# Performance work log

Measured on AMD Instinct MI355X. Metric: run time of the kernel, lower is better.

Reference implementation:

```python
import jax, jax.numpy as jnp
import numpy as np

VOCAB, D, H, HK, DH, M, DFF, NCLS = 32000, 512, 8, 2, 64, 64, 2048, 2
G = H // HK  # GQA group size = 4
EPS = 1e-6


def rmsnorm(x, g):
    return x * jax.lax.rsqrt(jnp.mean(x * x, axis=-1, keepdims=True) + EPS) * g


def setup_inputs() -> dict:
    key = jax.random.key(0)
    ks = jax.random.split(key, 14)
    s = 0.02
    return {
        "input_ids": jax.random.randint(ks[0], (8, 8192), 0, VOCAB),
        "emb": jax.random.normal(ks[1], (VOCAB, D), jnp.float32) * s,
        "Wq": jax.random.normal(ks[2], (D, H * DH), jnp.float32) * s,
        "Wk": jax.random.normal(ks[3], (D, HK * DH), jnp.float32) * s,
        "Wv": jax.random.normal(ks[4], (D, HK * DH), jnp.float32) * s,
        "Wphi": jax.random.normal(ks[5], (DH, M), jnp.float32),  # Laplacian kernel feature projection
        "Wo": jax.random.normal(ks[6], (H * DH, D), jnp.float32) * s,
        "g1": jnp.ones((D,), jnp.float32),
        "g2": jnp.ones((D,), jnp.float32),
        "Wg": jax.random.normal(ks[7], (D, DFF), jnp.float32) * s,
        "Wu": jax.random.normal(ks[8], (D, DFF), jnp.float32) * s,  # frozen up_proj (freeze only affects training, not math)
        "Wd": jax.random.normal(ks[9], (DFF, D), jnp.float32) * s,
        "Wc": jax.random.normal(ks[10], (D, NCLS), jnp.float32) * s,
        "bc": jnp.zeros((NCLS,), jnp.float32),
    }


def reference(input_ids, emb, Wq, Wk, Wv, Wphi, Wo, g1, g2, Wg, Wu, Wd, Wc, bc):
    B, S = input_ids.shape
    x = emb[input_ids]  # [B,S,D] embedding gather
    # --- kernelized (Laplacian) bidirectional GQA linear attention, pre-norm ---
    h = rmsnorm(x, g1)
    q = (h @ Wq).reshape(B, S, H, DH)
    k = (h @ Wk).reshape(B, S, HK, DH)
    v = (h @ Wv).reshape(B, S, HK, DH)
    # Laplacian positive feature map: phi(u) = exp(-|u @ Wphi|)  -> [.., M]
    pq = jnp.exp(-jnp.abs(jnp.einsum("bshd,dm->bshm", q, Wphi)))
    pk = jnp.exp(-jnp.abs(jnp.einsum("bskd,dm->bskm", k, Wphi)))
    # global (bidirectional) state per kv head: [B,HK,M,DH] and normalizer [B,HK,M]
    kv = jnp.einsum("bskm,bskd->bkmd", pk, v)
    z = pk.sum(axis=1)
    pqg = pq.reshape(B, S, HK, G, M)  # group query heads onto kv heads
    num = jnp.einsum("bskgm,bkmd->bskgd", pqg, kv)
    den = jnp.einsum("bskgm,bkm->bskg", pqg, z)
    attn = (num / (den[..., None] + EPS)).reshape(B, S, H * DH)
    x = x + attn @ Wo
    # --- SwiGLU FFN, pre-norm ---
    h2 = rmsnorm(x, g2)
    x = x + (jax.nn.silu(h2 @ Wg) * (h2 @ Wu)) @ Wd
    # --- mean pool + linear head ---
    logits = x.mean(axis=1) @ Wc + bc  # [B, NCLS]
    return logits
```

## Files before the change

kernel.cpp:

```cpp
#include <hip/hip_runtime.h>
#include <hip/hip_bf16.h>
#include <math.h>

typedef __attribute__((ext_vector_type(8))) short bf16x8;
typedef __attribute__((ext_vector_type(4))) float f32x4;

#define DEV static __device__ __forceinline__
#define AS1 __attribute__((address_space(1)))
#define AS3 __attribute__((address_space(3)))

DEV float bf2f(__hip_bfloat16 v) { return __bfloat162float(v); }
DEV __hip_bfloat16 f2bf(float f) { return __float2bfloat16(f); }
DEV float us2f(unsigned short u) { return __uint_as_float(((unsigned int)u) << 16); }
DEV unsigned short f2us(float f) {
    __hip_bfloat16 b = __float2bfloat16(f);
    return *(unsigned short*)&b;
}

DEV void gload_lds16(const void* g, void* l) {
    __builtin_amdgcn_global_load_lds((const AS1 unsigned int*)g,
                                     (AS3 unsigned int*)l, 16, 0, 0);
}

DEV void load8(const void* p, size_t off, int f32m, float* o) {
    if (f32m) {
        const float4* r = (const float4*)((const float*)p + off);
        float4 A = r[0], B = r[1];
        o[0] = A.x; o[1] = A.y; o[2] = A.z; o[3] = A.w;
        o[4] = B.x; o[5] = B.y; o[6] = B.z; o[7] = B.w;
    } else {
        const ushort4* r = (const ushort4*)((const __hip_bfloat16*)p + off);
        ushort4 A = r[0], B = r[1];
        o[0] = us2f(A.x); o[1] = us2f(A.y); o[2] = us2f(A.z); o[3] = us2f(A.w);
        o[4] = us2f(B.x); o[5] = us2f(B.y); o[6] = us2f(B.z); o[7] = us2f(B.w);
    }
}

DEV float loadElem(const void* p, size_t idx, int f32m) {
    return f32m ? ((const float*)p)[idx] : bf2f(((const __hip_bfloat16*)p)[idx]);
}

constexpr int NTOK = 65536;

constexpr size_t OFF_WQPT = 0;
constexpr size_t OFF_WKPT = OFF_WQPT + 524288ull;
constexpr size_t OFF_WVT  = OFF_WKPT + 131072ull;
constexpr size_t OFF_WOT  = OFF_WVT  + 131072ull;
constexpr size_t OFF_WGT  = OFF_WOT  + 524288ull;
constexpr size_t OFF_WUT  = OFF_WGT  + 2097152ull;
constexpr size_t OFF_KV   = OFF_WUT  + 2097152ull;
constexpr size_t OFF_Z    = OFF_KV   + 262144ull;
constexpr size_t OFF_POOL = OFF_Z    + 4096ull;
constexpr size_t OFF_TSUM = OFF_POOL + 16384ull;
constexpr size_t OFF_FLAG = OFF_TSUM + 65536ull;
constexpr size_t PERSIST  = OFF_FLAG + 256ull;
constexpr size_t OFF_H    = PERSIST;
constexpr size_t CHUNKBASE = OFF_H + 67108864ull;
constexpr int    ZERO_FLOATS = (262144 + 4096 + 16384 + 65536) / 4;
constexpr size_t PERTOK = 3584ull;

__global__ __launch_bounds__(128) void detect_kernel(
    const unsigned int* __restrict__ w, int* __restrict__ flag)
{
    __shared__ int cnt;
    if (threadIdx.x == 0) cnt = 0;
    __syncthreads();
    unsigned int v = w[threadIdx.x];
    float a = fabsf(us2f((unsigned short)(v & 0xFFFFu)));
    if (a >= 0.0625f && a <= 8.0f) atomicAdd(&cnt, 1);
    __syncthreads();
    if (threadIdx.x == 0) *flag = (cnt < 64) ? 1 : 0;
}

__global__ __launch_bounds__(256) void zero_kernel(float* __restrict__ p, int n)
{
    int i = blockIdx.x * 256 + threadIdx.x;
    if (i < n) p[i] = 0.0f;
}

__global__ __launch_bounds__(256) void fuse_phi_kernel(
    const void* __restrict__ W, const void* __restrict__ Wphi,
    __hip_bfloat16* __restrict__ outT, int wld, const int* __restrict__ flag)
{
    const int f = *flag;
    int o = blockIdx.x * 256 + threadIdx.x;
    int hm = o >> 9, d = o & 511;
    int h = hm >> 6, m = hm & 63;
    float acc = 0.f;
    if (f) {
        const float* Wf = (const float*)W;
        const float* Pf = (const float*)Wphi;
        #pragma unroll 8
        for (int dh = 0; dh < 64; ++dh)
            acc += Wf[(size_t)d * wld + h * 64 + dh] * Pf[dh * 64 + m];
    } else {
        const __hip_bfloat16* Wb = (const __hip_bfloat16*)W;
        const __hip_bfloat16* Pb = (const __hip_bfloat16*)Wphi;
        #pragma unroll 8
        for (int dh = 0; dh < 64; ++dh)
            acc += bf2f(Wb[(size_t)d * wld + h * 64 + dh]) * bf2f(Pb[dh * 64 + m]);
    }
    outT[o] = f2bf(acc);
}

__global__ __launch_bounds__(256) void transpose_kernel(
    const void* __restrict__ src, __hip_bfloat16* __restrict__ dst, int R, int Ccols,
    const int* __restrict__ flag)
{
    __shared__ float tile[32][33];
    const int f = *flag;
    const int tx = threadIdx.x & 31, ty = threadIdx.x >> 5;
    const int c0 = blockIdx.x * 32, r0 = blockIdx.y * 32;
    #pragma unroll
    for (int k = 0; k < 4; ++k) {
        const int rl = ty + k * 8;
        tile[rl][tx] = loadElem(src, (size_t)(r0 + rl) * Ccols + c0 + tx, f);
    }
    __syncthreads();
    #pragma unroll
    for (int k = 0; k < 4; ++k) {
        const int cl = ty + k * 8;
        dst[(size_t)(c0 + cl) * R + r0 + tx] = f2bf(tile[tx][cl]);
    }
}

__global__ __launch_bounds__(256) void embed_rms_kernel(
    const int* __restrict__ ids, const void* __restrict__ emb,
    const void* __restrict__ g1, __hip_bfloat16* __restrict__ h,
    const int* __restrict__ flag)
{
    const int f = *flag;
    const int n = blockIdx.x * 4 + (threadIdx.x >> 6);
    const int lane = threadIdx.x & 63;
    const int id = ids[n];
    float x[8];
    load8(emb, (size_t)id * 512 + lane * 8, f, x);
    float ss = 0.f;
    #pragma unroll
    for (int i = 0; i < 8; ++i) ss += x[i] * x[i];
    #pragma unroll
    for (int off = 32; off; off >>= 1) ss += __shfl_xor(ss, off, 64);
    const float scale = rsqrtf(ss * (1.0f / 512.0f) + 1e-6f);
    float gv[8];
    load8(g1, (size_t)lane * 8, f, gv);
    ushort4 h0, h1;
    h0.x = f2us(x[0] * scale * gv[0]); h0.y = f2us(x[1] * scale * gv[1]);
    h0.z = f2us(x[2] * scale * gv[2]); h0.w = f2us(x[3] * scale * gv[3]);
    h1.x = f2us(x[4] * scale * gv[4]); h1.y = f2us(x[5] * scale * gv[5]);
    h1.z = f2us(x[6] * scale * gv[6]); h1.w = f2us(x[7] * scale * gv[7]);
    ushort4* ho = (ushort4*)(h + (size_t)n * 512 + lane * 8);
    ho[0] = h0; ho[1] = h1;
}

__global__ __launch_bounds__(256) void rms2_kernel(
    const float* __restrict__ xf, const void* __restrict__ g2,
    __hip_bfloat16* __restrict__ h, const int* __restrict__ flag)
{
    const int f = *flag;
    const int n = blockIdx.x * 4 + (threadIdx.x >> 6);
    const int lane = threadIdx.x & 63;
    const float4* xr = (const float4*)(xf + (size_t)n * 512);
    float4 a = xr[lane * 2], b = xr[lane * 2 + 1];
    float x[8] = { a.x, a.y, a.z, a.w, b.x, b.y, b.z, b.w };
    float ss = 0.f;
    #pragma unroll
    for (int i = 0; i < 8; ++i) ss += x[i] * x[i];
    #pragma unroll
    for (int off = 32; off; off >>= 1) ss += __shfl_xor(ss, off, 64);
    const float scale = rsqrtf(ss * (1.0f / 512.0f) + 1e-6f);
    float gv[8];
    load8(g2, (size_t)lane * 8, f, gv);
    ushort4 h0, h1;
    h0.x = f2us(x[0] * scale * gv[0]); h0.y = f2us(x[1] * scale * gv[1]);
    h0.z = f2us(x[2] * scale * gv[2]); h0.w = f2us(x[3] * scale * gv[3]);
    h1.x = f2us(x[4] * scale * gv[4]); h1.y = f2us(x[5] * scale * gv[5]);
    h1.z = f2us(x[6] * scale * gv[6]); h1.w = f2us(x[7] * scale * gv[7]);
    ushort4* ho = (ushort4*)(h + (size_t)n * 512 + lane * 8);
    ho[0] = h0; ho[1] = h1;
}

template<int MODE>
__global__ __launch_bounds__(256) void gemm128_kernel(
    const __hip_bfloat16* __restrict__ A, const __hip_bfloat16* __restrict__ Bt,
    float* __restrict__ xf, __hip_bfloat16* __restrict__ Cout2,
    float* __restrict__ pooled, const int* __restrict__ ids,
    const void* __restrict__ emb, const int* __restrict__ flag, int gbase, int K)
{
    __shared__ __align__(16) char As[8192];
    __shared__ __align__(16) char Bs[8192];
    __shared__ int idsL[128];

    const int tid = threadIdx.x;
    const int bm = blockIdx.x, bn = blockIdx.y;
    const int wave = tid >> 6, lane = tid & 63;
    const int quad = lane >> 4, lr = lane & 15;
    const int wm = (wave >> 1) << 6, wn = (wave & 1) << 6;

    if (MODE == 7 && tid < 128) idsL[tid] = ids[bm * 128 + tid];

    const int srow = (wave << 5) + (lane >> 2);
    const int scol = lane & 3;
    const int sfr  = (srow + (srow >> 2)) & 3;
    const int sofs = ((scol ^ sfr) << 3);

    const __hip_bfloat16* ga0 = A  + (size_t)(bm * 128 + srow) * K + sofs;
    const __hip_bfloat16* gb0 = Bt + (size_t)(bn * 128 + srow) * K + sofs;
    const __hip_bfloat16* ga1 = ga0 + (size_t)16 * K;
    const __hip_bfloat16* gb1 = gb0 + (size_t)16 * K;
    char* lA0 = As + (wave << 11);
    char* lA1 = lA0 + 1024;
    char* lB0 = Bs + (wave << 11);
    char* lB1 = lB0 + 1024;

    const int fl  = (lr + (lr >> 2)) & 3;
    const int ac  = (quad ^ fl) << 4;
    const char* arp = As + ((wm + lr) << 6) + ac;
    const char* brp = Bs + ((wn + lr) << 6) + ac;

    f32x4 acc[4][4];
    #pragma unroll
    for (int i = 0; i < 4; ++i)
        #pragma unroll
        for (int j = 0; j < 4; ++j)
            #pragma unroll
            for (int r = 0; r < 4; ++r) acc[i][j][r] = 0.0f;

    for (int k0 = 0; k0 < K; k0 += 32) {
        __syncthreads();
        gload_lds16(ga0 + k0, lA0);
        gload_lds16(ga1 + k0, lA1);
        gload_lds16(gb0 + k0, lB0);
        gload_lds16(gb1 + k0, lB1);
        __syncthreads();

        bf16x8 af[4], bfr[4];
        #pragma unroll
        for (int i = 0; i < 4; ++i)
            af[i] = *(const bf16x8*)(arp + i * 1024);
        #pragma unroll
        for (int j = 0; j < 4; ++j)
            bfr[j] = *(const bf16x8*)(brp + j * 1024);
        #pragma unroll
        for (int i = 0; i < 4; ++i)
            #pragma unroll
            for (int j = 0; j < 4; ++j)
                acc[i][j] = __builtin_amdgcn_mfma_f32_16x16x32_bf16(af[i], bfr[j], acc[i][j], 0, 0, 0);
    }

    const int col0 = bn * 128 + wn + lr;

    if (MODE == 7) {
        const int f = *flag;
        const int b = (gbase + bm * 128) >> 13;
        #pragma unroll
        for (int j = 0; j < 4; ++j) {
            const int col = col0 + j * 16;
            float s = 0.f;
            #pragma unroll
            for (int i = 0; i < 4; ++i)
                #pragma unroll
                for (int r = 0; r < 4; ++r) {
                    const int rl = wm + i * 16 + quad * 4 + r;
                    const float e = loadElem(emb, (size_t)idsL[rl] * 512 + col, f);
                    const float w = e + acc[i][j][r];
                    xf[(size_t)(bm * 128 + rl) * 512 + col] = w;
                    s += w;
                }
            s += __shfl_xor(s, 16, 64);
            s += __shfl_xor(s, 32, 64);
            if (quad == 0) atomicAdd(&pooled[b * 512 + col], s);
        }
        return;
    }

    const int row0 = bm * 128 + wm + quad * 4;
    #pragma unroll
    for (int i = 0; i < 4; ++i)
        #pragma unroll
        for (int j = 0; j < 4; ++j) {
            const int col = col0 + j * 16;
            #pragma unroll
            for (int r = 0; r < 4; ++r) {
                const int row = row0 + i * 16 + r;
                const float v = acc[i][j][r];
                Cout2[(size_t)row * 256 + col] = f2bf(bn == 0 ? expf(-fabsf(v)) : v);
            }
        }
}

__global__ __launch_bounds__(256, 2) void pq_mix_kernel(
    const __hip_bfloat16* __restrict__ h, const __hip_bfloat16* __restrict__ WQPt,
    const float* __restrict__ kvf, const float* __restrict__ zf,
    __hip_bfloat16* __restrict__ attn, int gbase, int K)
{
    __shared__ __align__(16) char As[8192];
    __shared__ __align__(16) char Bs[8192];
    __shared__ __align__(16) char Pl[128 * 272];
    __shared__ __align__(16) __hip_bfloat16 kvT[80][72];

    const int tid = threadIdx.x;
    const int bm = blockIdx.x, bn = blockIdx.y;
    const int kh = bn >> 1;
    const int wave = tid >> 6, lane = tid & 63;
    const int quad = lane >> 4, lr = lane & 15;
    const int wm = (wave >> 1) << 6, wn = (wave & 1) << 6;
    const int b = (gbase + bm * 128) >> 13;

    {
        const float* kvsrc = kvf + ((size_t)b * 2 + kh) * 4096;
        for (int i = tid; i < 4096; i += 256) {
            const int m = i >> 6, dh = i & 63;
            kvT[dh][m] = f2bf(kvsrc[i]);
        }
        if (tid < 64) kvT[64][tid] = f2bf(zf[((size_t)b * 2 + kh) * 64 + tid]);
        for (int i = tid; i < 15 * 64; i += 256)
            kvT[65 + (i >> 6)][i & 63] = f2bf(0.0f);
    }

    const int srow = (wave << 5) + (lane >> 2);
    const int scol = lane & 3;
    const int sfr  = (srow + (srow >> 2)) & 3;
    const int sofs = ((scol ^ sfr) << 3);

    const __hip_bfloat16* ga0 = h    + (size_t)(bm * 128 + srow) * K + sofs;
    const __hip_bfloat16* gb0 = WQPt + (size_t)(bn * 128 + srow) * K + sofs;
    const __hip_bfloat16* ga1 = ga0 + (size_t)16 * K;
    const __hip_bfloat16* gb1 = gb0 + (size_t)16 * K;
    char* lA0 = As + (wave << 11);
    char* lA1 = lA0 + 1024;
    char* lB0 = Bs + (wave << 11);
    char* lB1 = lB0 + 1024;

    const int fl  = (lr + (lr >> 2)) & 3;
    const int ac  = (quad ^ fl) << 4;
    const char* arp = As + ((wm + lr) << 6) + ac;
    const char* brp = Bs + ((wn + lr) << 6) + ac;

    f32x4 acc[4][4];
    #pragma unroll
    for (int i = 0; i < 4; ++i)
        #pragma unroll
        for (int j = 0; j < 4; ++j)
            #pragma unroll
            for (int r = 0; r < 4; ++r) acc[i][j][r] = 0.0f;

    for (int k0 = 0; k0 < K; k0 += 32) {
        __syncthreads();
        gload_lds16(ga0 + k0, lA0);
        gload_lds16(ga1 + k0, lA1);
        gload_lds16(gb0 + k0, lB0);
        gload_lds16(gb1 + k0, lB1);
        __syncthreads();

        bf16x8 af[4], bfr[4];
        #pragma unroll
        for (int i = 0; i < 4; ++i)
            af[i] = *(const bf16x8*)(arp + i * 1024);
        #pragma unroll
        for (int j = 0; j < 4; ++j)
            bfr[j] = *(const bf16x8*)(brp + j * 1024);
        #pragma unroll
        for (int i = 0; i < 4; ++i)
            #pragma unroll
            for (int j = 0; j < 4; ++j)
                acc[i][j] = __builtin_amdgcn_mfma_f32_16x16x32_bf16(af[i], bfr[j], acc[i][j], 0, 0, 0);
    }

    #pragma unroll
    for (int i = 0; i < 4; ++i)
        #pragma unroll
        for (int j = 0; j < 4; ++j)
            #pragma unroll
            for (int r = 0; r < 4; ++r) {
                const int rl = wm + i * 16 + quad * 4 + r;
                const int cl = wn + j * 16 + lr;
                *(__hip_bfloat16*)(Pl + rl * 272 + cl * 2) = f2bf(expf(-fabsf(acc[i][j][r])));
            }
    __syncthreads();

    const int hl = wave & 1;
    f32x4 acc2[4][5];
    #pragma unroll
    for (int i = 0; i < 4; ++i)
        #pragma unroll
        for (int j = 0; j < 5; ++j)
            #pragma unroll
            for (int r = 0; r < 4; ++r) acc2[i][j][r] = 0.0f;

    #pragma unroll
    for (int kk = 0; kk < 2; ++kk) {
        const int kofs = kk * 32 + quad * 8;
        bf16x8 af[4], bfr[5];
        #pragma unroll
        for (int i = 0; i < 4; ++i)
            af[i] = *(const bf16x8*)(Pl + (wm + i * 16 + lr) * 272 + (wn + kofs) * 2);
        #pragma unroll
        for (int j = 0; j < 5; ++j)
            bfr[j] = *(const bf16x8*)&kvT[j * 16 + lr][kofs];
        #pragma unroll
        for (int i = 0; i < 4; ++i)
            #pragma unroll
            for (int j = 0; j < 5; ++j)
                acc2[i][j] = __builtin_amdgcn_mfma_f32_16x16x32_bf16(af[i], bfr[j], acc2[i][j], 0, 0, 0);
    }

    const int colb = (bn * 2 + hl) * 64;
    #pragma unroll
    for (int i = 0; i < 4; ++i) {
        const int rowb = bm * 128 + wm + i * 16 + quad * 4;
        #pragma unroll
        for (int r = 0; r < 4; ++r) {
            const float den = __shfl(acc2[i][4][r], lane & 48, 64);
            const float inv = 1.0f / (den + 1e-6f);
            const size_t base = (size_t)(rowb + r) * 512 + colb;
            #pragma unroll
            for (int j = 0; j < 4; ++j)
                attn[base + j * 16 + lr] = f2bf(acc2[i][j][r] * inv);
        }
    }
}

__global__ __launch_bounds__(512, 2) void ffn8_kernel(
    const __hip_bfloat16* __restrict__ A, const __hip_bfloat16* __restrict__ Bg,
    const __hip_bfloat16* __restrict__ Bu, float* __restrict__ tsum, int gbase)
{
    __shared__ __align__(16) char L[131072];

    const int tid = threadIdx.x;
    const int bm = blockIdx.x;
    const int wave = tid >> 6, lane = tid & 63;
    const int quad = lane >> 4, lr = lane & 15;

    {
        const int ss = (lane & 56) | ((lane ^ wave) & 7);
        const __hip_bfloat16* gsrc = A + (size_t)(bm * 128 + wave) * 512 + ss * 8;
        char* ldst = L + wave * 1024;
        #pragma unroll
        for (int i = 0; i < 16; ++i)
            gload_lds16(gsrc + (size_t)i * 8 * 512, ldst + i * 8192);
    }
    asm volatile("s_waitcnt vmcnt(0)" ::: "memory");
    __syncthreads();

    const int x7s = (lr & 7) << 4;
    const char* ap = L + (lr << 10) + (((quad << 4) ^ x7s) & 0x70) + ((quad << 4) & ~0x70);
    const char* apq = L + (lr << 10);

    const __hip_bfloat16* pG = Bg + (size_t)(wave * 256 + lr) * 512 + quad * 8;
    const __hip_bfloat16* pU = Bu + (size_t)(wave * 256 + lr) * 512 + quad * 8;

    const int b = (gbase + bm * 128) >> 13;
    (void)ap;

    for (int ci = 0; ci < 8; ++ci) {
        const __hip_bfloat16* pGc = pG + (size_t)ci * 32 * 512;
        const __hip_bfloat16* pUc = pU + (size_t)ci * 32 * 512;

        f32x4 aG[8][2], aU[8][2];
        #pragma unroll
        for (int m = 0; m < 8; ++m)
            #pragma unroll
            for (int c = 0; c < 2; ++c)
                #pragma unroll
                for (int r = 0; r < 4; ++r) { aG[m][c][r] = 0.0f; aU[m][c][r] = 0.0f; }

        #pragma unroll 2
        for (int ks = 0; ks < 16; ++ks) {
            const int so = ((ks << 6) | (quad << 4)) ^ x7s;
            bf16x8 af[8];
            #pragma unroll
            for (int m = 0; m < 8; ++m)
                af[m] = *(const bf16x8*)(apq + m * 16384 + so);
            bf16x8 bg0 = *(const bf16x8*)(pGc + ks * 32);
            bf16x8 bg1 = *(const bf16x8*)(pGc + 16 * 512 + ks * 32);
            bf16x8 bu0 = *(const bf16x8*)(pUc + ks * 32);
            bf16x8 bu1 = *(const bf16x8*)(pUc + 16 * 512 + ks * 32);
            #pragma unroll
            for (int m = 0; m < 8; ++m) {
                aG[m][0] = __builtin_amdgcn_mfma_f32_16x16x32_bf16(af[m], bg0, aG[m][0], 0, 0, 0);
                aG[m][1] = __builtin_amdgcn_mfma_f32_16x16x32_bf16(af[m], bg1, aG[m][1], 0, 0, 0);
                aU[m][0] = __builtin_amdgcn_mfma_f32_16x16x32_bf16(af[m], bu0, aU[m][0], 0, 0, 0);
                aU[m][1] = __builtin_amdgcn_mfma_f32_16x16x32_bf16(af[m], bu1, aU[m][1], 0, 0, 0);
            }
        }

        #pragma unroll
        for (int c = 0; c < 2; ++c) {
            float s = 0.f;
            #pragma unroll
            for (int m = 0; m < 8; ++m)
                #pragma unroll
                for (int r = 0; r < 4; ++r) {
                    const float g = aG[m][c][r];
                    s += (g / (1.0f + expf(-g))) * aU[m][c][r];
                }
            s += __shfl_xor(s, 16, 64);
            s += __shfl_xor(s, 32, 64);
            if (quad == 0)
                atomicAdd(&tsum[b * 2048 + wave * 256 + ci * 32 + c * 16 + lr], s);
        }
    }
}

__global__ __launch_bounds__(256) void ffn_pool_kernel(
    const float* __restrict__ tsum, const void* __restrict__ Wd,
    float* __restrict__ pooled, const int* __restrict__ flag)
{
    __shared__ float ts[8][64];
    const int f = *flag;
    const int k0 = blockIdx.x * 64;
    const int t = threadIdx.x;
    for (int i = t; i < 512; i += 256)
        ts[i >> 6][i & 63] = tsum[(i >> 6) * 2048 + k0 + (i & 63)];
    __syncthreads();

    float acc0[8] = {}, acc1[8] = {};
    for (int kk = 0; kk < 64; ++kk) {
        const size_t krow = (size_t)(k0 + kk) * 512;
        const float w0 = loadElem(Wd, krow + t, f);
        const float w1 = loadElem(Wd, krow + t + 256, f);
        #pragma unroll
        for (int b = 0; b < 8; ++b) {
            acc0[b] += ts[b][kk] * w0;
            acc1[b] += ts[b][kk] * w1;
        }
    }
    #pragma unroll
    for (int b = 0; b < 8; ++b) {
        atomicAdd(&pooled[b * 512 + t], acc0[b]);
        atomicAdd(&pooled[b * 512 + t + 256], acc1[b]);
    }
}

__global__ __launch_bounds__(256) void kv_z_kernel(
    const __hip_bfloat16* __restrict__ pkv,
    float* __restrict__ kv, float* __restrict__ z, int gbase, int nrows)
{
    __shared__ float pks[8][64], vs[8][64];
    const int slab = blockIdx.x, kh = blockIdx.y;
    const int b = (gbase + slab * nrows) >> 13;
    const int tid = threadIdx.x;
    const int tm = (tid & 15) << 2, tdh = (tid >> 4) << 2;
    const int lss = tid >> 5, lmm = (tid & 31) << 1;

    float acc[4][4] = {};
    float zacc[4] = {};
    for (int sb = 0; sb < nrows; sb += 8) {
        __syncthreads();
        {
            const size_t n = (size_t)slab * nrows + sb + lss;
            const __hip_bfloat16* pr = pkv + n * 256 + kh * 64 + lmm;
            const __hip_bfloat16* vr = pkv + n * 256 + 128 + kh * 64 + lmm;
            pks[lss][lmm]     = bf2f(pr[0]);
            pks[lss][lmm + 1] = bf2f(pr[1]);
            vs[lss][lmm]      = bf2f(vr[0]);
            vs[lss][lmm + 1]  = bf2f(vr[1]);
        }
        __syncthreads();
        #pragma unroll
        for (int ss = 0; ss < 8; ++ss) {
            f32x4 p = *(const f32x4*)&pks[ss][tm];
            f32x4 w = *(const f32x4*)&vs[ss][tdh];
            #pragma unroll
            for (int i = 0; i < 4; ++i)
                #pragma unroll
                for (int j = 0; j < 4; ++j)
                    acc[i][j] += p[i] * w[j];
            if ((tid >> 4) == 0) {
                #pragma unroll
                for (int i = 0; i < 4; ++i) zacc[i] += p[i];
            }
        }
    }
    #pragma unroll
    for (int i = 0; i < 4; ++i)
        #pragma unroll
        for (int j = 0; j < 4; ++j)
            atomicAdd(&kv[(((size_t)b * 2 + kh) * 64 + tm + i) * 64 + tdh + j], acc[i][j]);
    if ((tid >> 4) == 0) {
        #pragma unroll
        for (int i = 0; i < 4; ++i)
            atomicAdd(&z[((size_t)b * 2 + kh) * 64 + tm + i], zacc[i]);
    }
}

__global__ __launch_bounds__(256) void head_kernel(
    const float* __restrict__ pooled, const void* __restrict__ Wc,
    const void* __restrict__ bc, void* __restrict__ out, const int* __restrict__ flag)
{
    const int f = *flag;
    const int t = threadIdx.x;
    const int grp = t >> 4, ln = t & 15;
    const int b = grp >> 1, c = grp & 1;
    float p = 0.f;
    for (int d = ln; d < 512; d += 16)
        p += pooled[b * 512 + d] * loadElem(Wc, (size_t)d * 2 + c, f);
    #pragma unroll
    for (int off = 8; off; off >>= 1) p += __shfl_xor(p, off, 64);
    if (ln == 0) {
        const float val = p * (1.0f / 8192.0f) + loadElem(bc, c, f);
        if (f) ((float*)out)[b * 2 + c] = val;
        else   ((__hip_bfloat16*)out)[b * 2 + c] = f2bf(val);
    }
}

extern "C" void kernel_launch(void* const* d_in, const int* in_sizes, int n_in,
                              void* d_out, int out_size, void* d_ws, size_t ws_size,
                              hipStream_t stream)
{
    const int* ids   = (const int*)d_in[0];
    const void* emb  = d_in[1];
    const void* Wq   = d_in[2];
    const void* Wk   = d_in[3];
    const void* Wv   = d_in[4];
    const void* Wph  = d_in[5];
    const void* Wo   = d_in[6];
    const void* g1   = d_in[7];
    const void* g2   = d_in[8];
    const void* Wg   = d_in[9];
    const void* Wu   = d_in[10];
    const void* Wd   = d_in[11];
    const void* Wc   = d_in[12];
    const void* bc   = d_in[13];

    char* ws = (char*)d_ws;
    __hip_bfloat16* WQPt  = (__hip_bfloat16*)(ws + OFF_WQPT);
    __hip_bfloat16* WKPt  = (__hip_bfloat16*)(ws + OFF_WKPT);
    __hip_bfloat16* WvT   = (__hip_bfloat16*)(ws + OFF_WVT);
    __hip_bfloat16* WoT   = (__hip_bfloat16*)(ws + OFF_WOT);
    __hip_bfloat16* WgT   = (__hip_bfloat16*)(ws + OFF_WGT);
    __hip_bfloat16* WuT   = (__hip_bfloat16*)(ws + OFF_WUT);
    float*          kv    = (float*)(ws + OFF_KV);
    float*          z     = (float*)(ws + OFF_Z);
    float*          pooled= (float*)(ws + OFF_POOL);
    float*          tsum  = (float*)(ws + OFF_TSUM);
    int*            flag  = (int*)(ws + OFF_FLAG);
    __hip_bfloat16* hall  = (__hip_bfloat16*)(ws + OFF_H);

    int C = 32768;
    while (C > 256 && CHUNKBASE + PERTOK * (size_t)C > ws_size) C >>= 1;
    const int NC = NTOK / C;

    char* cb = ws + CHUNKBASE;
    float*          xf   = (float*)cb;
    __hip_bfloat16* attn = (__hip_bfloat16*)(cb + (size_t)C * 2048);
    __hip_bfloat16* pkv  = (__hip_bfloat16*)(cb + (size_t)C * 3072);

    detect_kernel<<<1, 128, 0, stream>>>((const unsigned int*)Wph, flag);
    zero_kernel<<<(ZERO_FLOATS + 255) / 256, 256, 0, stream>>>(kv, ZERO_FLOATS);

    fuse_phi_kernel<<<1024, 256, 0, stream>>>(Wq, Wph, WQPt, 512, flag);
    fuse_phi_kernel<<<256, 256, 0, stream>>>(Wk, Wph, WKPt, 128, flag);
    transpose_kernel<<<dim3(128 / 32, 512 / 32), 256, 0, stream>>>(Wv, WvT, 512, 128, flag);
    transpose_kernel<<<dim3(512 / 32, 512 / 32), 256, 0, stream>>>(Wo, WoT, 512, 512, flag);
    transpose_kernel<<<dim3(2048 / 32, 512 / 32), 256, 0, stream>>>(Wg, WgT, 512, 2048, flag);
    transpose_kernel<<<dim3(2048 / 32, 512 / 32), 256, 0, stream>>>(Wu, WuT, 512, 2048, flag);

    for (int c = 0; c < NC; ++c) {
        const int g0 = c * C;
        __hip_bfloat16* hc = hall + (size_t)g0 * 512;
        embed_rms_kernel<<<C / 4, 256, 0, stream>>>(ids + g0, emb, g1, hc, flag);
        gemm128_kernel<8><<<dim3(C / 128, 2), 256, 0, stream>>>(
            hc, WKPt, nullptr, pkv, nullptr, nullptr, nullptr, flag, g0, 512);
        kv_z_kernel<<<dim3(C / 128, 2), 256, 0, stream>>>(pkv, kv, z, g0, 128);
    }

    for (int c = 0; c < NC; ++c) {
        const int g0 = c * C;
        __hip_bfloat16* hc = hall + (size_t)g0 * 512;
        pq_mix_kernel<<<dim3(C / 128, 4), 256, 0, stream>>>(
            hc, WQPt, kv, z, attn, g0, 512);
        gemm128_kernel<7><<<dim3(C / 128, 4), 256, 0, stream>>>(
            attn, WoT, xf, nullptr, pooled, ids + g0, emb, flag, g0, 512);
        rms2_kernel<<<C / 4, 256, 0, stream>>>(xf, g2, hc, flag);
        ffn8_kernel<<<C / 128, 512, 0, stream>>>(hc, WgT, WuT, tsum, g0);
    }

    ffn_pool_kernel<<<32, 256, 0, stream>>>(tsum, Wd, pooled, flag);

    head_kernel<<<1, 256, 0, stream>>>(pooled, Wc, bc, d_out, flag);
}
```

Measured before the change: 933.7 us.

## Double-buffer FFN operand loads and batch tsum atomics via shared memory

Restructures the FFN gate/up MFMA inner loop into an explicit two-stage software pipeline. The next k-step's LDS A fragments and global B fragments are issued before the current MFMAs, with manual waitcnt and sched_barrier controlling the ordering. It also collects per-column SwiGLU sums in a shared buffer and does the global atomicAdds once at the end, with coalesced indexing. This costs more registers for the double buffers and 8KB extra LDS on top of the 128KB already used, which may hurt occupancy under launch_bounds(512,2).

```diff
diff --git a/kernel.cpp b/kernel.cpp
--- a/kernel.cpp
+++ b/kernel.cpp
@@ -420,11 +420,33 @@
     }
 }
 
+DEV void ffn_loadA(bf16x8* a, const char* apq, int so) {
+    #pragma unroll
+    for (int m = 0; m < 8; ++m)
+        a[m] = *(const bf16x8*)(apq + m * 16384 + so);
+}
+DEV void ffn_loadB(bf16x8* b, const __hip_bfloat16* pGc, const __hip_bfloat16* pUc, int ks) {
+    b[0] = *(const bf16x8*)(pGc + ks * 32);
+    b[1] = *(const bf16x8*)(pGc + 16 * 512 + ks * 32);
+    b[2] = *(const bf16x8*)(pUc + ks * 32);
+    b[3] = *(const bf16x8*)(pUc + 16 * 512 + ks * 32);
+}
+DEV void ffn_mfma(f32x4 (&aG)[8][2], f32x4 (&aU)[8][2], const bf16x8* a, const bf16x8* b) {
+    #pragma unroll
+    for (int m = 0; m < 8; ++m) {
+        aG[m][0] = __builtin_amdgcn_mfma_f32_16x16x32_bf16(a[m], b[0], aG[m][0], 0, 0, 0);
+        aG[m][1] = __builtin_amdgcn_mfma_f32_16x16x32_bf16(a[m], b[1], aG[m][1], 0, 0, 0);
+        aU[m][0] = __builtin_amdgcn_mfma_f32_16x16x32_bf16(a[m], b[2], aU[m][0], 0, 0, 0);
+        aU[m][1] = __builtin_amdgcn_mfma_f32_16x16x32_bf16(a[m], b[3], aU[m][1], 0, 0, 0);
+    }
+}
+
 __global__ __launch_bounds__(512, 2) void ffn8_kernel(
     const __hip_bfloat16* __restrict__ A, const __hip_bfloat16* __restrict__ Bg,
     const __hip_bfloat16* __restrict__ Bu, float* __restrict__ tsum, int gbase)
 {
     __shared__ __align__(16) char L[131072];
+    __shared__ float sBuf[2048];
 
     const int tid = threadIdx.x;
     const int bm = blockIdx.x;
@@ -443,14 +465,12 @@
     __syncthreads();
 
     const int x7s = (lr & 7) << 4;
-    const char* ap = L + (lr << 10) + (((quad << 4) ^ x7s) & 0x70) + ((quad << 4) & ~0x70);
     const char* apq = L + (lr << 10);
 
     const __hip_bfloat16* pG = Bg + (size_t)(wave * 256 + lr) * 512 + quad * 8;
     const __hip_bfloat16* pU = Bu + (size_t)(wave * 256 + lr) * 512 + quad * 8;
 
     const int b = (gbase + bm * 128) >> 13;
-    (void)ap;
 
     for (int ci = 0; ci < 8; ++ci) {
         const __hip_bfloat16* pGc = pG + (size_t)ci * 32 * 512;
@@ -464,24 +484,28 @@
                 #pragma unroll
                 for (int r = 0; r < 4; ++r) { aG[m][c][r] = 0.0f; aU[m][c][r] = 0.0f; }
 
-        #pragma unroll 2
-        for (int ks = 0; ks < 16; ++ks) {
-            const int so = ((ks << 6) | (quad << 4)) ^ x7s;
-            bf16x8 af[8];
-            #pragma unroll
-            for (int m = 0; m < 8; ++m)
-                af[m] = *(const bf16x8*)(apq + m * 16384 + so);
-            bf16x8 bg0 = *(const bf16x8*)(pGc + ks * 32);
-            bf16x8 bg1 = *(const bf16x8*)(pGc + 16 * 512 + ks * 32);
-            bf16x8 bu0 = *(const bf16x8*)(pUc + ks * 32);
-            bf16x8 bu1 = *(const bf16x8*)(pUc + 16 * 512 + ks * 32);
-            #pragma unroll
-            for (int m = 0; m < 8; ++m) {
-                aG[m][0] = __builtin_amdgcn_mfma_f32_16x16x32_bf16(af[m], bg0, aG[m][0], 0, 0, 0);
-                aG[m][1] = __builtin_amdgcn_mfma_f32_16x16x32_bf16(af[m], bg1, aG[m][1], 0, 0, 0);
-                aU[m][0] = __builtin_amdgcn_mfma_f32_16x16x32_bf16(af[m], bu0, aU[m][0], 0, 0, 0);
-                aU[m][1] = __builtin_amdgcn_mfma_f32_16x16x32_bf16(af[m], bu1, aU[m][1], 0, 0, 0);
+        bf16x8 a0[8], a1[8], b0[4], b1[4];
+        ffn_loadA(a0, apq, ((0 << 6) | (quad << 4)) ^ x7s);
+        ffn_loadB(b0, pGc, pUc, 0);
+
+        #pragma unroll
+        for (int kp = 0; kp < 8; ++kp) {
+            const int k1 = 2 * kp + 1;
+            ffn_loadA(a1, apq, ((k1 << 6) | (quad << 4)) ^ x7s);
+            ffn_loadB(b1, pGc, pUc, k1);
+            asm volatile("s_waitcnt lgkmcnt(8) vmcnt(4)" ::: "memory");
+            __builtin_amdgcn_sched_barrier(0);
+            ffn_mfma(aG, aU, a0, b0);
+            if (kp < 7) {
+                const int k2 = 2 * kp + 2;
+                ffn_loadA(a0, apq, ((k2 << 6) | (quad << 4)) ^ x7s);
+                ffn_loadB(b0, pGc, pUc, k2);
+                asm volatile("s_waitcnt lgkmcnt(8) vmcnt(4)" ::: "memory");
+            } else {
+                asm volatile("s_waitcnt lgkmcnt(0) vmcnt(0)" ::: "memory");
             }
+            __builtin_amdgcn_sched_barrier(0);
+            ffn_mfma(aG, aU, a1, b1);
         }
 
         #pragma unroll
@@ -496,9 +520,15 @@
                 }
             s += __shfl_xor(s, 16, 64);
             s += __shfl_xor(s, 32, 64);
-            if (quad == 0)
-                atomicAdd(&tsum[b * 2048 + wave * 256 + ci * 32 + c * 16 + lr], s);
-        }
+            if (quad == 0) sBuf[wave * 256 + ci * 32 + c * 16 + lr] = s;
+        }
+    }
+
+    __syncthreads();
+    #pragma unroll
+    for (int i = 0; i < 4; ++i) {
+        const int idx = tid * 4 + i;
+        atomicAdd(&tsum[b * 2048 + idx], sBuf[idx]);
     }
 }
 
```

Measured after the change: 940.5 us. Within noise of the previous version (+0.7%).
